# Performance work log

Measured on AMD Instinct MI355X. Metric: run time of the kernel, lower is better.

## Reference

```python
import jax, jax.numpy as jnp
import numpy as np

N = 50000   # nodes
E = 800000  # edges
D = 64      # num_filters == hidden_channels
NG = 5      # num_gaussians (edge_attr width, unused by forward math)
NEG_SLOPE = 0.2


def setup_inputs() -> dict:
    key = jax.random.key(0)
    ks = jax.random.split(key, 16)
    s = 1.0 / np.sqrt(D)
    return {
        "x": jax.random.normal(ks[0], (N, D), dtype=jnp.float32),
        "edge_index": jax.random.randint(ks[1], (2, E), 0, N, dtype=jnp.int64),
        "edge_weight": jax.random.uniform(ks[2], (E,), dtype=jnp.float32),
        "edge_attr": jax.random.normal(ks[3], (E, NG), dtype=jnp.float32),
        "W0": jax.random.normal(ks[4], (D, D), dtype=jnp.float32) * s,
        "b0": jnp.zeros((D,), dtype=jnp.float32),
        "W1": jax.random.normal(ks[5], (D, D), dtype=jnp.float32) * s,
        "as1": jax.random.normal(ks[6], (D,), dtype=jnp.float32) * s,
        "ad1": jax.random.normal(ks[7], (D,), dtype=jnp.float32) * s,
        "b1": jnp.zeros((D,), dtype=jnp.float32),
        "W2": jax.random.normal(ks[8], (D, D), dtype=jnp.float32) * s,
        "as2": jax.random.normal(ks[9], (D,), dtype=jnp.float32) * s,
        "ad2": jax.random.normal(ks[10], (D,), dtype=jnp.float32) * s,
        "b2": jnp.zeros((D,), dtype=jnp.float32),
    }


def gat_layer(h, src, dst, W, a_src, a_dst, b):
    # PyG GATConv, heads=1, add_self_loops=False
    hx = h @ W  # [N, D]
    # per-node attention logits, gathered per edge (edge j->i: src=j, dst=i)
    alpha = (hx * a_src).sum(-1)[src] + (hx * a_dst).sum(-1)[dst]  # [E]
    alpha = jax.nn.leaky_relu(alpha, NEG_SLOPE)
    # segment softmax grouped by destination node
    m = jax.ops.segment_max(alpha, dst, num_segments=N)
    e = jnp.exp(alpha - m[dst])
    s = jax.ops.segment_sum(e, dst, num_segments=N)
    p = e / s[dst]  # [E]
    # scatter-add weighted source features
    out = jax.ops.segment_sum(hx[src] * p[:, None], dst, num_segments=N)
    return out + b


def reference(x, edge_index, edge_weight, edge_attr,
              W0, b0, W1, as1, ad1, b1, W2, as2, ad2, b2):
    # edge_weight / edge_attr are accepted but unused, as in the torch module
    src, dst = edge_index[0], edge_index[1]
    out = jax.nn.relu(x @ W0 + b0)
    out = out + jax.nn.relu(gat_layer(out, src, dst, W1, as1, ad1, b1))
    out = out + jax.nn.relu(gat_layer(out, src, dst, W2, as2, ad2, b2))
    return out
```

## Files before the change

kernel.cpp:

```cpp
#include <hip/hip_runtime.h>
#include <hip/hip_bf16.h>

#define DD 64
#define NEG_SLOPE 0.2f
#define HS 68
#define BSH 8
#define BN  256
#define NBMAX 256
#define NBLK 256
#define STAGE_CAP 6144

__device__ __forceinline__ unsigned short f2bf(float f)
{
    unsigned u = __float_as_uint(f);
    u += 0x7FFFu + ((u >> 16) & 1u);
    return (unsigned short)(u >> 16);
}

__device__ __forceinline__ int wave_incl_scan(int v, int lane)
{
#pragma unroll
    for (int off = 1; off < 64; off <<= 1) {
        int t = __shfl_up(v, off);
        if (lane >= off) v += t;
    }
    return v;
}

__global__ __launch_bounds__(256) void k1_count_mm(
    const int4* __restrict__ dst4, const int* __restrict__ dst,
    int* __restrict__ cnts, int NB, int E4, int E, int C4,
    const float* __restrict__ x,
    const float* __restrict__ W0, const float* __restrict__ b0,
    const float* __restrict__ W1,
    const float* __restrict__ a_src, const float* __restrict__ a_dst,
    float* __restrict__ h, ushort4* __restrict__ hxb4,
    float* __restrict__ sarr, float* __restrict__ darr, int n)
{
    __shared__ float Wsh[DD * DD];
    __shared__ float Hsh[DD * HS];
    int tid = threadIdx.x;

    if (blockIdx.x < NBLK) {
        int* lh = (int*)Wsh;
        int k = blockIdx.x;
        for (int i = tid; i < NB; i += 256) lh[i] = 0;
        __syncthreads();
        int i0 = k * C4, i1 = min(i0 + C4, E4);
        for (int i = i0 + tid; i < i1; i += 256) {
            int4 d = dst4[i];
            atomicAdd(&lh[d.x >> BSH], 1);
            atomicAdd(&lh[d.y >> BSH], 1);
            atomicAdd(&lh[d.z >> BSH], 1);
            atomicAdd(&lh[d.w >> BSH], 1);
        }
        if (k == NBLK - 1) {
            for (int e = E4 * 4 + tid; e < E; e += 256)
                atomicAdd(&lh[dst[e] >> BSH], 1);
        }
        __syncthreads();
        for (int i = tid; i < NB; i += 256) cnts[k * NB + i] = lh[i];
        return;
    }

    for (int i = tid * 4; i < DD * DD; i += 1024)
        *(float4*)&Wsh[i] = *(const float4*)&W0[i];

    int fg = tid & 15, ng = tid >> 4;
    int tile0 = (blockIdx.x - NBLK) * 64;
    for (int p = 0; p < 4; ++p) {
        int nl = p * 16 + ng, gn = tile0 + nl;
        if (gn < n)
            *(float4*)&Hsh[nl * HS + 4 * fg] = *(const float4*)&x[gn * DD + 4 * fg];
    }
    __syncthreads();

    float4 acc[4];
#pragma unroll
    for (int j = 0; j < 4; ++j) acc[j] = float4{0.f, 0.f, 0.f, 0.f};
#pragma unroll 8
    for (int k = 0; k < DD; ++k) {
        float4 w4 = *(float4*)&Wsh[k * DD + 4 * fg];
#pragma unroll
        for (int j = 0; j < 4; ++j) {
            float hv = Hsh[(4 * ng + j) * HS + k];
            acc[j].x += hv * w4.x; acc[j].y += hv * w4.y;
            acc[j].z += hv * w4.z; acc[j].w += hv * w4.w;
        }
    }

    float4 b4 = *(const float4*)&b0[4 * fg];
    float4 o[4];
#pragma unroll
    for (int j = 0; j < 4; ++j) {
        o[j].x = fmaxf(acc[j].x + b4.x, 0.f);
        o[j].y = fmaxf(acc[j].y + b4.y, 0.f);
        o[j].z = fmaxf(acc[j].z + b4.z, 0.f);
        o[j].w = fmaxf(acc[j].w + b4.w, 0.f);
        int gn = tile0 + 4 * ng + j;
        if (gn < n) *(float4*)&h[gn * DD + 4 * fg] = o[j];
    }
    __syncthreads();

#pragma unroll
    for (int j = 0; j < 4; ++j)
        *(float4*)&Hsh[(4 * ng + j) * HS + 4 * fg] = o[j];
    for (int i = tid * 4; i < DD * DD; i += 1024)
        *(float4*)&Wsh[i] = *(const float4*)&W1[i];
    __syncthreads();

#pragma unroll
    for (int j = 0; j < 4; ++j) acc[j] = float4{0.f, 0.f, 0.f, 0.f};
#pragma unroll 8
    for (int k = 0; k < DD; ++k) {
        float4 w4 = *(float4*)&Wsh[k * DD + 4 * fg];
#pragma unroll
        for (int j = 0; j < 4; ++j) {
            float hv = Hsh[(4 * ng + j) * HS + k];
            acc[j].x += hv * w4.x; acc[j].y += hv * w4.y;
            acc[j].z += hv * w4.z; acc[j].w += hv * w4.w;
        }
    }

    float4 as4 = *(const float4*)&a_src[4 * fg];
    float4 ad4 = *(const float4*)&a_dst[4 * fg];
#pragma unroll
    for (int j = 0; j < 4; ++j) {
        int gn = tile0 + 4 * ng + j;
        if (gn < n) {
            ushort4 hb;
            hb.x = f2bf(acc[j].x); hb.y = f2bf(acc[j].y);
            hb.z = f2bf(acc[j].z); hb.w = f2bf(acc[j].w);
            hxb4[gn * 16 + fg] = hb;
        }
        float ps = acc[j].x * as4.x + acc[j].y * as4.y + acc[j].z * as4.z + acc[j].w * as4.w;
        float pd = acc[j].x * ad4.x + acc[j].y * ad4.y + acc[j].z * ad4.z + acc[j].w * ad4.w;
#pragma unroll
        for (int off = 8; off; off >>= 1) {
            ps += __shfl_xor(ps, off);
            pd += __shfl_xor(pd, off);
        }
        if (fg == 0 && gn < n) { sarr[gn] = ps; darr[gn] = pd; }
    }
}

__global__ __launch_bounds__(256) void mm_gat(
    const float* __restrict__ h, const float* __restrict__ W,
    const float* __restrict__ a_src, const float* __restrict__ a_dst,
    ushort4* __restrict__ hxb4, float* __restrict__ sarr, float* __restrict__ darr,
    int n)
{
    __shared__ float Wsh[DD * DD];
    __shared__ float Hsh[DD * HS];
    int tid = threadIdx.x;
    for (int i = tid * 4; i < DD * DD; i += 1024)
        *(float4*)&Wsh[i] = *(const float4*)&W[i];

    int fg = tid & 15, ng = tid >> 4;
    int tile0 = blockIdx.x * 64;
    for (int p = 0; p < 4; ++p) {
        int nl = p * 16 + ng, gn = tile0 + nl;
        if (gn < n)
            *(float4*)&Hsh[nl * HS + 4 * fg] = *(const float4*)&h[gn * DD + 4 * fg];
    }
    __syncthreads();

    float4 acc[4];
#pragma unroll
    for (int j = 0; j < 4; ++j) acc[j] = float4{0.f, 0.f, 0.f, 0.f};
#pragma unroll 8
    for (int k = 0; k < DD; ++k) {
        float4 w4 = *(float4*)&Wsh[k * DD + 4 * fg];
#pragma unroll
        for (int j = 0; j < 4; ++j) {
            float hv = Hsh[(4 * ng + j) * HS + k];
            acc[j].x += hv * w4.x; acc[j].y += hv * w4.y;
            acc[j].z += hv * w4.z; acc[j].w += hv * w4.w;
        }
    }

    float4 as4 = *(const float4*)&a_src[4 * fg];
    float4 ad4 = *(const float4*)&a_dst[4 * fg];
#pragma unroll
    for (int j = 0; j < 4; ++j) {
        int gn = tile0 + 4 * ng + j;
        if (gn < n) {
            ushort4 hb;
            hb.x = f2bf(acc[j].x); hb.y = f2bf(acc[j].y);
            hb.z = f2bf(acc[j].z); hb.w = f2bf(acc[j].w);
            hxb4[gn * 16 + fg] = hb;
        }
        float ps = acc[j].x * as4.x + acc[j].y * as4.y + acc[j].z * as4.z + acc[j].w * as4.w;
        float pd = acc[j].x * ad4.x + acc[j].y * ad4.y + acc[j].z * ad4.z + acc[j].w * ad4.w;
#pragma unroll
        for (int off = 8; off; off >>= 1) {
            ps += __shfl_xor(ps, off);
            pd += __shfl_xor(pd, off);
        }
        if (fg == 0 && gn < n) { sarr[gn] = ps; darr[gn] = pd; }
    }
}

__global__ __launch_bounds__(512) void k2_scan_scatter(
    const int* __restrict__ cnts,
    const int4* __restrict__ dst4, const int4* __restrict__ src4,
    const int* __restrict__ dst, const int* __restrict__ src,
    int* __restrict__ boff, int* __restrict__ row_ptr, int* __restrict__ ebuf,
    int NB, int N, int E, int E4, int C4)
{
    __shared__ int lcur[NBMAX];
    __shared__ int stot[NBMAX];
    __shared__ int wsum[4];
    int k = blockIdx.x, tid = threadIdx.x;

    int mybase = 0, tot = 0;
    if (tid < NB) {
        for (int kk = 0; kk < NBLK; ++kk) {
            int c = cnts[kk * NB + tid];
            tot += c;
            mybase += (kk < k) ? c : 0;
        }
        stot[tid] = tot;
    }
    __syncthreads();

    int lane = tid & 63, w = tid >> 6;
    int incl = 0, v = 0;
    if (tid < 256) {
        v = (tid < NB) ? stot[tid] : 0;
        incl = wave_incl_scan(v, lane);
        if (lane == 63) wsum[w] = incl;
    }
    __syncthreads();
    if (tid < NB) {
        int wo = 0;
        for (int i = 0; i < w; ++i) wo += wsum[i];
        int excl = wo + incl - v;
        lcur[tid] = excl + mybase;
        if (k == 0) {
            boff[tid] = excl;
            if (tid == 0) { boff[NB] = E; row_ptr[N] = E; }
        }
    }
    __syncthreads();

    int i0 = k * C4, i1 = min(i0 + C4, E4);
    for (int i = i0 + tid; i < i1; i += 512) {
        int4 d = dst4[i];
        int4 s = src4[i];
        int b, p;
        b = d.x >> BSH; p = atomicAdd(&lcur[b], 1); ebuf[p] = ((d.x & (BN - 1)) << 24) | s.x;
        b = d.y >> BSH; p = atomicAdd(&lcur[b], 1); ebuf[p] = ((d.y & (BN - 1)) << 24) | s.y;
        b = d.z >> BSH; p = atomicAdd(&lcur[b], 1); ebuf[p] = ((d.z & (BN - 1)) << 24) | s.z;
        b = d.w >> BSH; p = atomicAdd(&lcur[b], 1); ebuf[p] = ((d.w & (BN - 1)) << 24) | s.w;
    }
    if (k == NBLK - 1) {
        for (int e = E4 * 4 + tid; e < E; e += 512) {
            int d = dst[e];
            int b = d >> BSH;
            int p = atomicAdd(&lcur[b], 1);
            ebuf[p] = ((d & (BN - 1)) << 24) | src[e];
        }
    }
}

__global__ __launch_bounds__(512) void group_build(
    const int* __restrict__ ebuf, const int* __restrict__ boff,
    int* __restrict__ row_ptr, int* __restrict__ col, int N)
{
    __shared__ int lcnt[BN];
    __shared__ int loff[BN];
    __shared__ int lcur[BN];
    __shared__ int wsum[4];
    __shared__ int stage[STAGE_CAP];
    int b = blockIdx.x, tid = threadIdx.x;
    int e0 = boff[b], e1 = boff[b + 1];
    int total = e1 - e0;
    if (tid < BN) { lcnt[tid] = 0; lcur[tid] = 0; }
    __syncthreads();
    for (int e = e0 + tid; e < e1; e += 512)
        atomicAdd(&lcnt[((unsigned)ebuf[e]) >> 24], 1);
    __syncthreads();
    int lane = tid & 63, w = tid >> 6;
    int v = (tid < BN) ? lcnt[tid] : 0;
    int incl = wave_incl_scan(v, lane);
    if (tid < BN && lane == 63) wsum[w] = incl;
    __syncthreads();
    if (tid < BN) {
        int wo = 0;
        for (int i = 0; i < w; ++i) wo += wsum[i];
        int excl = wo + incl - v;
        loff[tid] = excl;
        int node = b * BN + tid;
        if (node < N) row_ptr[node] = e0 + excl;
    }
    __syncthreads();
    if (total <= STAGE_CAP) {
        for (int e = e0 + tid; e < e1; e += 512) {
            int p = ebuf[e];
            int dl = ((unsigned)p) >> 24;
            int r = atomicAdd(&lcur[dl], 1);
            stage[loff[dl] + r] = p & 0xFFFFFF;
        }
        __syncthreads();
        for (int i = tid; i < total; i += 512)
            col[e0 + i] = stage[i];
    } else {
        for (int e = e0 + tid; e < e1; e += 512) {
            int p = ebuf[e];
            int dl = ((unsigned)p) >> 24;
            int r = atomicAdd(&lcur[dl], 1);
            col[e0 + loff[dl] + r] = p & 0xFFFFFF;
        }
    }
}

__device__ __forceinline__ void agg_node(
    int node, int deg, const int* __restrict__ colp,
    const uint4* __restrict__ hxq, const float* __restrict__ sarr,
    float adi, const float* __restrict__ bias, float* __restrict__ h,
    int lane, int fl, int es)
{
    float acc[8];
#pragma unroll
    for (int j = 0; j < 8; ++j) acc[j] = 0.f;
    float inv = 0.f;

    if (deg > 0 && deg <= 64) {
        int c = 0; float a = -3.4e38f;
        if (lane < deg) {
            c = colp[lane];
            a = sarr[c] + adi;
            a = a > 0.f ? a : NEG_SLOPE * a;
        }
        float m = a;
#pragma unroll
        for (int off = 32; off; off >>= 1) m = fmaxf(m, __shfl_xor(m, off));
        float wgt = (lane < deg) ? __expf(a - m) : 0.f;
        float s = wgt;
#pragma unroll
        for (int off = 32; off; off >>= 1) s += __shfl_xor(s, off);
        inv = 1.f / s;

        for (int base = 0; base < deg; base += 8) {
            int e = base + es;
            float we = __shfl(wgt, e);
            int ce = __shfl(c, e);
            if (we > 0.f) {
                uint4 u = hxq[(size_t)ce * 8 + fl];
                acc[0] += we * __uint_as_float(u.x << 16);
                acc[1] += we * __uint_as_float(u.x & 0xffff0000u);
                acc[2] += we * __uint_as_float(u.y << 16);
                acc[3] += we * __uint_as_float(u.y & 0xffff0000u);
                acc[4] += we * __uint_as_float(u.z << 16);
                acc[5] += we * __uint_as_float(u.z & 0xffff0000u);
                acc[6] += we * __uint_as_float(u.w << 16);
                acc[7] += we * __uint_as_float(u.w & 0xffff0000u);
            }
        }
#pragma unroll
        for (int off = 8; off < 64; off <<= 1) {
#pragma unroll
            for (int j = 0; j < 8; ++j) acc[j] += __shfl_xor(acc[j], off);
        }
    } else if (deg > 64) {
        float m = -3.4e38f, s = 0.f;
        for (int e = es; e < deg; e += 8) {
            int cc = colp[e];
            float a = sarr[cc] + adi;
            a = a > 0.f ? a : NEG_SLOPE * a;
            uint4 u = hxq[(size_t)cc * 8 + fl];
            float mN = fmaxf(m, a);
            float f = __expf(m - mN);
            float wg = __expf(a - mN);
            m = mN; s = s * f + wg;
            acc[0] = acc[0] * f + wg * __uint_as_float(u.x << 16);
            acc[1] = acc[1] * f + wg * __uint_as_float(u.x & 0xffff0000u);
            acc[2] = acc[2] * f + wg * __uint_as_float(u.y << 16);
            acc[3] = acc[3] * f + wg * __uint_as_float(u.y & 0xffff0000u);
            acc[4] = acc[4] * f + wg * __uint_as_float(u.z << 16);
            acc[5] = acc[5] * f + wg * __uint_as_float(u.z & 0xffff0000u);
            acc[6] = acc[6] * f + wg * __uint_as_float(u.w << 16);
            acc[7] = acc[7] * f + wg * __uint_as_float(u.w & 0xffff0000u);
        }
#pragma unroll
        for (int off = 8; off < 64; off <<= 1) {
            float m2 = __shfl_xor(m, off);
            float s2 = __shfl_xor(s, off);
            float mN = fmaxf(m, m2);
            float f1 = __expf(m - mN);
            float f2 = __expf(m2 - mN);
            s = s * f1 + s2 * f2;
#pragma unroll
            for (int j = 0; j < 8; ++j) {
                float a2 = __shfl_xor(acc[j], off);
                acc[j] = acc[j] * f1 + a2 * f2;
            }
            m = mN;
        }
        inv = (s > 0.f) ? 1.f / s : 0.f;
    }

    if (es == 0) {
        float* hp = &h[(size_t)node * DD + fl * 8];
        float4 c0 = *(float4*)hp;
        float4 c1 = *(float4*)(hp + 4);
        const float* bp = &bias[fl * 8];
        float4 b0 = *(const float4*)bp;
        float4 b1 = *(const float4*)(bp + 4);
        c0.x += fmaxf(acc[0] * inv + b0.x, 0.f);
        c0.y += fmaxf(acc[1] * inv + b0.y, 0.f);
        c0.z += fmaxf(acc[2] * inv + b0.z, 0.f);
        c0.w += fmaxf(acc[3] * inv + b0.w, 0.f);
        c1.x += fmaxf(acc[4] * inv + b1.x, 0.f);
        c1.y += fmaxf(acc[5] * inv + b1.y, 0.f);
        c1.z += fmaxf(acc[6] * inv + b1.z, 0.f);
        c1.w += fmaxf(acc[7] * inv + b1.w, 0.f);
        *(float4*)hp = c0;
        *(float4*)(hp + 4) = c1;
    }
}

__global__ __launch_bounds__(256) void aggregate(
    const uint4* __restrict__ hxq, const int* __restrict__ row_ptr,
    const int* __restrict__ col, const float* __restrict__ sarr,
    const float* __restrict__ darr, const float* __restrict__ bias,
    float* __restrict__ h, int n)
{
    int tid = threadIdx.x;
    int wid = tid >> 6, lane = tid & 63;
    int fl = lane & 7, es = lane >> 3;
    int v = blockIdx.x * 4 + wid;
    if (v >= n) return;
    int beg = row_ptr[v], end = row_ptr[v + 1];
    agg_node(v, end - beg, &col[beg], hxq, sarr, darr[v], bias, h, lane, fl, es);
}

extern "C" void kernel_launch(void* const* d_in, const int* in_sizes, int n_in,
                              void* d_out, int out_size, void* d_ws, size_t ws_size,
                              hipStream_t stream)
{
    const float* x  = (const float*)d_in[0];
    const int*   ei = (const int*)d_in[1];
    const float* W0 = (const float*)d_in[4];
    const float* b0 = (const float*)d_in[5];
    const float* W1 = (const float*)d_in[6];
    const float* as1= (const float*)d_in[7];
    const float* ad1= (const float*)d_in[8];
    const float* b1 = (const float*)d_in[9];
    const float* W2 = (const float*)d_in[10];
    const float* as2= (const float*)d_in[11];
    const float* ad2= (const float*)d_in[12];
    const float* b2 = (const float*)d_in[13];

    int N = in_sizes[0] / DD;
    int E = in_sizes[1] / 2;
    int E4 = E >> 2;
    int C4 = (E4 + NBLK - 1) / NBLK;
    int NB = (N + BN - 1) >> BSH;
    float* h = (float*)d_out;

    ushort4* hxb4 = (ushort4*)d_ws;
    float* sarr   = (float*)(hxb4 + (size_t)N * 16);
    float* darr   = sarr + N;
    int*   row_ptr= (int*)(darr + N);
    int*   cnts   = row_ptr + (N + 1);
    int*   boff   = cnts + NBLK * NB;
    int*   ebuf   = boff + (NB + 1);
    int*   colb   = ebuf + E;

    const int* src = ei;
    const int* dst = ei + E;
    const int4* dst4 = (const int4*)dst;
    const int4* src4 = (const int4*)src;

    int mm_tiles = (N + 63) / 64;
    int agg_blks = (N + 3) / 4;

    k1_count_mm<<<NBLK + mm_tiles, 256, 0, stream>>>(
        dst4, dst, cnts, NB, E4, E, C4,
        x, W0, b0, W1, as1, ad1, h, hxb4, sarr, darr, N);

    k2_scan_scatter<<<NBLK, 512, 0, stream>>>(
        cnts, dst4, src4, dst, src, boff, row_ptr, ebuf, NB, N, E, E4, C4);

    group_build<<<NB, 512, 0, stream>>>(ebuf, boff, row_ptr, colb, N);

    aggregate<<<agg_blks, 256, 0, stream>>>(
        (const uint4*)hxb4, row_ptr, colb, sarr, darr, b1, h, N);

    mm_gat<<<mm_tiles, 256, 0, stream>>>(h, W2, as2, ad2, hxb4, sarr, darr, N);
    aggregate<<<agg_blks, 256, 0, stream>>>(
        (const uint4*)hxb4, row_ptr, colb, sarr, darr, b2, h, N);
}
```

Before: 219.8 us.

## Quantize transformed node features to int8 with per-node scale for aggregation

The bf16 copy of the transformed features gathered per edge is replaced with int8 values plus one float scale per node, which halves the bytes fetched for each edge in the gather-heavy aggregation. The aggregation lane mapping changes to 16 edges by 4 feature lanes, with per-edge weights pre-multiplied by the source scale. The matmul inner loop is also restructured to use float4 LDS reads over k. The cost is lower precision, with int8 quantisation error that could exceed tolerance, plus extra shuffle-max and rounding work in the producer kernels.

```diff
diff --git a/kernel.cpp b/kernel.cpp
--- a/kernel.cpp
+++ b/kernel.cpp
@@ -10,13 +10,6 @@
 #define NBLK 256
 #define STAGE_CAP 6144
 
-__device__ __forceinline__ unsigned short f2bf(float f)
-{
-    unsigned u = __float_as_uint(f);
-    u += 0x7FFFu + ((u >> 16) & 1u);
-    return (unsigned short)(u >> 16);
-}
-
 __device__ __forceinline__ int wave_incl_scan(int v, int lane)
 {
 #pragma unroll
@@ -26,6 +19,40 @@
     }
     return v;
 }
+
+__device__ __forceinline__ void quant_store(
+    float4 a, int gn, int fg, unsigned* __restrict__ hxq8u,
+    float* __restrict__ scl, int n)
+{
+    float amax = fmaxf(fmaxf(fabsf(a.x), fabsf(a.y)), fmaxf(fabsf(a.z), fabsf(a.w)));
+#pragma unroll
+    for (int off = 1; off < 16; off <<= 1) amax = fmaxf(amax, __shfl_xor(amax, off));
+    float iq = (amax > 0.f) ? 127.f / amax : 0.f;
+    int q0 = (int)rintf(a.x * iq), q1 = (int)rintf(a.y * iq);
+    int q2 = (int)rintf(a.z * iq), q3 = (int)rintf(a.w * iq);
+    unsigned u = (q0 & 255) | ((q1 & 255) << 8) | ((q2 & 255) << 16) | ((q3 & 255) << 24);
+    if (gn < n) {
+        hxq8u[(size_t)gn * 16 + fg] = u;
+        if (fg == 0) scl[gn] = amax * (1.f / 127.f);
+    }
+}
+
+#define MM_INNER(ACC)                                                         \
+    _Pragma("unroll")                                                         \
+    for (int k4 = 0; k4 < DD / 4; ++k4) {                                     \
+        float4 w0 = *(float4*)&Wsh[(4 * k4 + 0) * DD + 4 * fg];               \
+        float4 w1 = *(float4*)&Wsh[(4 * k4 + 1) * DD + 4 * fg];               \
+        float4 w2 = *(float4*)&Wsh[(4 * k4 + 2) * DD + 4 * fg];               \
+        float4 w3 = *(float4*)&Wsh[(4 * k4 + 3) * DD + 4 * fg];               \
+        _Pragma("unroll")                                                     \
+        for (int j = 0; j < 4; ++j) {                                         \
+            float4 hv = *(float4*)&Hsh[(4 * ng + j) * HS + 4 * k4];           \
+            ACC[j].x += hv.x * w0.x + hv.y * w1.x + hv.z * w2.x + hv.w * w3.x;\
+            ACC[j].y += hv.x * w0.y + hv.y * w1.y + hv.z * w2.y + hv.w * w3.y;\
+            ACC[j].z += hv.x * w0.z + hv.y * w1.z + hv.z * w2.z + hv.w * w3.z;\
+            ACC[j].w += hv.x * w0.w + hv.y * w1.w + hv.z * w2.w + hv.w * w3.w;\
+        }                                                                     \
+    }
 
 __global__ __launch_bounds__(256) void k1_count_mm(
     const int4* __restrict__ dst4, const int* __restrict__ dst,
@@ -34,7 +61,7 @@
     const float* __restrict__ W0, const float* __restrict__ b0,
     const float* __restrict__ W1,
     const float* __restrict__ a_src, const float* __restrict__ a_dst,
-    float* __restrict__ h, ushort4* __restrict__ hxb4,
+    float* __restrict__ h, unsigned* __restrict__ hxq8u, float* __restrict__ scl,
     float* __restrict__ sarr, float* __restrict__ darr, int n)
 {
     __shared__ float Wsh[DD * DD];
@@ -78,16 +105,7 @@
     float4 acc[4];
 #pragma unroll
     for (int j = 0; j < 4; ++j) acc[j] = float4{0.f, 0.f, 0.f, 0.f};
-#pragma unroll 8
-    for (int k = 0; k < DD; ++k) {
-        float4 w4 = *(float4*)&Wsh[k * DD + 4 * fg];
-#pragma unroll
-        for (int j = 0; j < 4; ++j) {
-            float hv = Hsh[(4 * ng + j) * HS + k];
-            acc[j].x += hv * w4.x; acc[j].y += hv * w4.y;
-            acc[j].z += hv * w4.z; acc[j].w += hv * w4.w;
-        }
-    }
+    MM_INNER(acc)
 
     float4 b4 = *(const float4*)&b0[4 * fg];
     float4 o[4];
@@ -111,28 +129,14 @@
 
 #pragma unroll
     for (int j = 0; j < 4; ++j) acc[j] = float4{0.f, 0.f, 0.f, 0.f};
-#pragma unroll 8
-    for (int k = 0; k < DD; ++k) {
-        float4 w4 = *(float4*)&Wsh[k * DD + 4 * fg];
-#pragma unroll
-        for (int j = 0; j < 4; ++j) {
-            float hv = Hsh[(4 * ng + j) * HS + k];
-            acc[j].x += hv * w4.x; acc[j].y += hv * w4.y;
-            acc[j].z += hv * w4.z; acc[j].w += hv * w4.w;
-        }
-    }
+    MM_INNER(acc)
 
     float4 as4 = *(const float4*)&a_src[4 * fg];
     float4 ad4 = *(const float4*)&a_dst[4 * fg];
 #pragma unroll
     for (int j = 0; j < 4; ++j) {
         int gn = tile0 + 4 * ng + j;
-        if (gn < n) {
-            ushort4 hb;
-            hb.x = f2bf(acc[j].x); hb.y = f2bf(acc[j].y);
-            hb.z = f2bf(acc[j].z); hb.w = f2bf(acc[j].w);
-            hxb4[gn * 16 + fg] = hb;
-        }
+        quant_store(acc[j], gn, fg, hxq8u, scl, n);
         float ps = acc[j].x * as4.x + acc[j].y * as4.y + acc[j].z * as4.z + acc[j].w * as4.w;
         float pd = acc[j].x * ad4.x + acc[j].y * ad4.y + acc[j].z * ad4.z + acc[j].w * ad4.w;
 #pragma unroll
@@ -147,8 +151,8 @@
 __global__ __launch_bounds__(256) void mm_gat(
     const float* __restrict__ h, const float* __restrict__ W,
     const float* __restrict__ a_src, const float* __restrict__ a_dst,
-    ushort4* __restrict__ hxb4, float* __restrict__ sarr, float* __restrict__ darr,
-    int n)
+    unsigned* __restrict__ hxq8u, float* __restrict__ scl,
+    float* __restrict__ sarr, float* __restrict__ darr, int n)
 {
     __shared__ float Wsh[DD * DD];
     __shared__ float Hsh[DD * HS];
@@ -168,28 +172,14 @@
     float4 acc[4];
 #pragma unroll
     for (int j = 0; j < 4; ++j) acc[j] = float4{0.f, 0.f, 0.f, 0.f};
-#pragma unroll 8
-    for (int k = 0; k < DD; ++k) {
-        float4 w4 = *(float4*)&Wsh[k * DD + 4 * fg];
-#pragma unroll
-        for (int j = 0; j < 4; ++j) {
-            float hv = Hsh[(4 * ng + j) * HS + k];
-            acc[j].x += hv * w4.x; acc[j].y += hv * w4.y;
-            acc[j].z += hv * w4.z; acc[j].w += hv * w4.w;
-        }
-    }
+    MM_INNER(acc)
 
     float4 as4 = *(const float4*)&a_src[4 * fg];
     float4 ad4 = *(const float4*)&a_dst[4 * fg];
 #pragma unroll
     for (int j = 0; j < 4; ++j) {
         int gn = tile0 + 4 * ng + j;
-        if (gn < n) {
-            ushort4 hb;
-            hb.x = f2bf(acc[j].x); hb.y = f2bf(acc[j].y);
-            hb.z = f2bf(acc[j].z); hb.w = f2bf(acc[j].w);
-            hxb4[gn * 16 + fg] = hb;
-        }
+        quant_store(acc[j], gn, fg, hxq8u, scl, n);
         float ps = acc[j].x * as4.x + acc[j].y * as4.y + acc[j].z * as4.z + acc[j].w * as4.w;
         float pd = acc[j].x * ad4.x + acc[j].y * ad4.y + acc[j].z * ad4.z + acc[j].w * ad4.w;
 #pragma unroll
@@ -317,13 +307,14 @@
 
 __device__ __forceinline__ void agg_node(
     int node, int deg, const int* __restrict__ colp,
-    const uint4* __restrict__ hxq, const float* __restrict__ sarr,
-    float adi, const float* __restrict__ bias, float* __restrict__ h,
-    int lane, int fl, int es)
-{
-    float acc[8];
-#pragma unroll
-    for (int j = 0; j < 8; ++j) acc[j] = 0.f;
+    const uint4* __restrict__ hxq8, const float* __restrict__ scl,
+    const float* __restrict__ sarr, float adi,
+    const float* __restrict__ bias, float* __restrict__ h, int lane)
+{
+    int fl = lane & 3, es = lane >> 2;
+    float acc[16];
+#pragma unroll
+    for (int i = 0; i < 16; ++i) acc[i] = 0.f;
     float inv = 0.f;
 
     if (deg > 0 && deg <= 64) {
@@ -341,50 +332,71 @@
 #pragma unroll
         for (int off = 32; off; off >>= 1) s += __shfl_xor(s, off);
         inv = 1.f / s;
-
-        for (int base = 0; base < deg; base += 8) {
+        float wsc = (lane < deg) ? wgt * scl[c] : 0.f;
+
+        for (int base = 0; base < deg; base += 16) {
             int e = base + es;
-            float we = __shfl(wgt, e);
-            int ce = __shfl(c, e);
-            if (we > 0.f) {
-                uint4 u = hxq[(size_t)ce * 8 + fl];
-                acc[0] += we * __uint_as_float(u.x << 16);
-                acc[1] += we * __uint_as_float(u.x & 0xffff0000u);
-                acc[2] += we * __uint_as_float(u.y << 16);
-                acc[3] += we * __uint_as_float(u.y & 0xffff0000u);
-                acc[4] += we * __uint_as_float(u.z << 16);
-                acc[5] += we * __uint_as_float(u.z & 0xffff0000u);
-                acc[6] += we * __uint_as_float(u.w << 16);
-                acc[7] += we * __uint_as_float(u.w & 0xffff0000u);
+            float bw = __shfl(wsc, e);
+            int bc = __shfl(c, e);
+            if (bw != 0.f) {
+                uint4 u = hxq8[(size_t)bc * 4 + fl];
+                int t;
+                t = (int)(u.x << 24) >> 24; acc[0]  += bw * (float)t;
+                t = (int)(u.x << 16) >> 24; acc[1]  += bw * (float)t;
+                t = (int)(u.x <<  8) >> 24; acc[2]  += bw * (float)t;
+                t = (int)u.x >> 24;         acc[3]  += bw * (float)t;
+                t = (int)(u.y << 24) >> 24; acc[4]  += bw * (float)t;
+                t = (int)(u.y << 16) >> 24; acc[5]  += bw * (float)t;
+                t = (int)(u.y <<  8) >> 24; acc[6]  += bw * (float)t;
+                t = (int)u.y >> 24;         acc[7]  += bw * (float)t;
+                t = (int)(u.z << 24) >> 24; acc[8]  += bw * (float)t;
+                t = (int)(u.z << 16) >> 24; acc[9]  += bw * (float)t;
+                t = (int)(u.z <<  8) >> 24; acc[10] += bw * (float)t;
+                t = (int)u.z >> 24;         acc[11] += bw * (float)t;
+                t = (int)(u.w << 24) >> 24; acc[12] += bw * (float)t;
+                t = (int)(u.w << 16) >> 24; acc[13] += bw * (float)t;
+                t = (int)(u.w <<  8) >> 24; acc[14] += bw * (float)t;
+                t = (int)u.w >> 24;         acc[15] += bw * (float)t;
             }
         }
 #pragma unroll
-        for (int off = 8; off < 64; off <<= 1) {
-#pragma unroll
-            for (int j = 0; j < 8; ++j) acc[j] += __shfl_xor(acc[j], off);
+        for (int off = 4; off < 64; off <<= 1) {
+#pragma unroll
+            for (int i = 0; i < 16; ++i) acc[i] += __shfl_xor(acc[i], off);
         }
     } else if (deg > 64) {
         float m = -3.4e38f, s = 0.f;
-        for (int e = es; e < deg; e += 8) {
-            int cc = colp[e];
-            float a = sarr[cc] + adi;
+        for (int e = es; e < deg; e += 16) {
+            int c = colp[e];
+            float a = sarr[c] + adi;
             a = a > 0.f ? a : NEG_SLOPE * a;
-            uint4 u = hxq[(size_t)cc * 8 + fl];
+            float sc = scl[c];
+            uint4 u = hxq8[(size_t)c * 4 + fl];
             float mN = fmaxf(m, a);
             float f = __expf(m - mN);
             float wg = __expf(a - mN);
             m = mN; s = s * f + wg;
-            acc[0] = acc[0] * f + wg * __uint_as_float(u.x << 16);
-            acc[1] = acc[1] * f + wg * __uint_as_float(u.x & 0xffff0000u);
-            acc[2] = acc[2] * f + wg * __uint_as_float(u.y << 16);
-            acc[3] = acc[3] * f + wg * __uint_as_float(u.y & 0xffff0000u);
-            acc[4] = acc[4] * f + wg * __uint_as_float(u.z << 16);
-            acc[5] = acc[5] * f + wg * __uint_as_float(u.z & 0xffff0000u);
-            acc[6] = acc[6] * f + wg * __uint_as_float(u.w << 16);
-            acc[7] = acc[7] * f + wg * __uint_as_float(u.w & 0xffff0000u);
-        }
-#pragma unroll
-        for (int off = 8; off < 64; off <<= 1) {
+            float wq = wg * sc;
+            int t;
+            t = (int)(u.x << 24) >> 24; acc[0]  = acc[0]  * f + wq * (float)t;
+            t = (int)(u.x << 16) >> 24; acc[1]  = acc[1]  * f + wq * (float)t;
+            t = (int)(u.x <<  8) >> 24; acc[2]  = acc[2]  * f + wq * (float)t;
+            t = (int)u.x >> 24;         acc[3]  = acc[3]  * f + wq * (float)t;
+            t = (int)(u.y << 24) >> 24; acc[4]  = acc[4]  * f + wq * (float)t;
+            t = (int)(u.y << 16) >> 24; acc[5]  = acc[5]  * f + wq * (float)t;
+            t = (int)(u.y <<  8) >> 24; acc[6]  = acc[6]  * f + wq * (float)t;
+            t = (int)u.y >> 24;         acc[7]  = acc[7]  * f + wq * (float)t;
+            t = (int)(u.z << 24) >> 24; acc[8]  = acc[8]  * f + wq * (float)t;
+            t = (int)(u.z << 16) >> 24; acc[9]  = acc[9]  * f + wq * (float)t;
+            t = (int)(u.z <<  8) >> 24; acc[10] = acc[10] * f + wq * (float)t;
+            t = (int)u.z >> 24;         acc[11] = acc[11] * f + wq * (float)t;
+            t = (int)(u.w << 24) >> 24; acc[12] = acc[12] * f + wq * (float)t;
+            t = (int)(u.w << 16) >> 24; acc[13] = acc[13] * f + wq * (float)t;
+            t = (int)(u.w <<  8) >> 24; acc[14] = acc[14] * f + wq * (float)t;
+            t = (int)u.w >> 24;         acc[15] = acc[15] * f + wq * (float)t;
+        }
+#pragma unroll
+        for (int off = 4; off < 64; off <<= 1) {
             float m2 = __shfl_xor(m, off);
             float s2 = __shfl_xor(s, off);
             float mN = fmaxf(m, m2);
@@ -392,9 +404,9 @@
             float f2 = __expf(m2 - mN);
             s = s * f1 + s2 * f2;
 #pragma unroll
-            for (int j = 0; j < 8; ++j) {
-                float a2 = __shfl_xor(acc[j], off);
-                acc[j] = acc[j] * f1 + a2 * f2;
+            for (int i = 0; i < 16; ++i) {
+                float a2 = __shfl_xor(acc[i], off);
+                acc[i] = acc[i] * f1 + a2 * f2;
             }
             m = mN;
         }
@@ -402,38 +414,33 @@
     }
 
     if (es == 0) {
-        float* hp = &h[(size_t)node * DD + fl * 8];
-        float4 c0 = *(float4*)hp;
-        float4 c1 = *(float4*)(hp + 4);
-        const float* bp = &bias[fl * 8];
-        float4 b0 = *(const float4*)bp;
-        float4 b1 = *(const float4*)(bp + 4);
-        c0.x += fmaxf(acc[0] * inv + b0.x, 0.f);
-        c0.y += fmaxf(acc[1] * inv + b0.y, 0.f);
-        c0.z += fmaxf(acc[2] * inv + b0.z, 0.f);
-        c0.w += fmaxf(acc[3] * inv + b0.w, 0.f);
-        c1.x += fmaxf(acc[4] * inv + b1.x, 0.f);
-        c1.y += fmaxf(acc[5] * inv + b1.y, 0.f);
-        c1.z += fmaxf(acc[6] * inv + b1.z, 0.f);
-        c1.w += fmaxf(acc[7] * inv + b1.w, 0.f);
-        *(float4*)hp = c0;
-        *(float4*)(hp + 4) = c1;
+        float* hp = &h[(size_t)node * DD + fl * 16];
+        const float* bp = &bias[fl * 16];
+#pragma unroll
+        for (int q = 0; q < 4; ++q) {
+            float4 cur = *(float4*)(hp + 4 * q);
+            float4 bb = *(const float4*)(bp + 4 * q);
+            cur.x += fmaxf(acc[4 * q + 0] * inv + bb.x, 0.f);
+            cur.y += fmaxf(acc[4 * q + 1] * inv + bb.y, 0.f);
+            cur.z += fmaxf(acc[4 * q + 2] * inv + bb.z, 0.f);
+            cur.w += fmaxf(acc[4 * q + 3] * inv + bb.w, 0.f);
+            *(float4*)(hp + 4 * q) = cur;
+        }
     }
 }
 
 __global__ __launch_bounds__(256) void aggregate(
-    const uint4* __restrict__ hxq, const int* __restrict__ row_ptr,
-    const int* __restrict__ col, const float* __restrict__ sarr,
-    const float* __restrict__ darr, const float* __restrict__ bias,
-    float* __restrict__ h, int n)
+    const uint4* __restrict__ hxq8, const float* __restrict__ scl,
+    const int* __restrict__ row_ptr, const int* __restrict__ col,
+    const float* __restrict__ sarr, const float* __restrict__ darr,
+    const float* __restrict__ bias, float* __restrict__ h, int n)
 {
     int tid = threadIdx.x;
     int wid = tid >> 6, lane = tid & 63;
-    int fl = lane & 7, es = lane >> 3;
     int v = blockIdx.x * 4 + wid;
     if (v >= n) return;
     int beg = row_ptr[v], end = row_ptr[v + 1];
-    agg_node(v, end - beg, &col[beg], hxq, sarr, darr[v], bias, h, lane, fl, es);
+    agg_node(v, end - beg, &col[beg], hxq8, scl, sarr, darr[v], bias, h, lane);
 }
 
 extern "C" void kernel_launch(void* const* d_in, const int* in_sizes, int n_in,
@@ -460,8 +467,9 @@
     int NB = (N + BN - 1) >> BSH;
     float* h = (float*)d_out;
 
-    ushort4* hxb4 = (ushort4*)d_ws;
-    float* sarr   = (float*)(hxb4 + (size_t)N * 16);
+    unsigned* hxq8u = (unsigned*)d_ws;
+    float* scl    = (float*)(hxq8u + (size_t)N * 16);
+    float* sarr   = scl + N;
     float* darr   = sarr + N;
     int*   row_ptr= (int*)(darr + N);
     int*   cnts   = row_ptr + (N + 1);
@@ -479,7 +487,7 @@
 
     k1_count_mm<<<NBLK + mm_tiles, 256, 0, stream>>>(
         dst4, dst, cnts, NB, E4, E, C4,
-        x, W0, b0, W1, as1, ad1, h, hxb4, sarr, darr, N);
+        x, W0, b0, W1, as1, ad1, h, hxq8u, scl, sarr, darr, N);
 
     k2_scan_scatter<<<NBLK, 512, 0, stream>>>(
         cnts, dst4, src4, dst, src, boff, row_ptr, ebuf, NB, N, E, E4, C4);
@@ -487,9 +495,9 @@
     group_build<<<NB, 512, 0, stream>>>(ebuf, boff, row_ptr, colb, N);
 
     aggregate<<<agg_blks, 256, 0, stream>>>(
-        (const uint4*)hxb4, row_ptr, colb, sarr, darr, b1, h, N);
-
-    mm_gat<<<mm_tiles, 256, 0, stream>>>(h, W2, as2, ad2, hxb4, sarr, darr, N);
+        (const uint4*)hxq8u, scl, row_ptr, colb, sarr, darr, b1, h, N);
+
+    mm_gat<<<mm_tiles, 256, 0, stream>>>(h, W2, as2, ad2, hxq8u, scl, sarr, darr, N);
     aggregate<<<agg_blks, 256, 0, stream>>>(
-        (const uint4*)hxb4, row_ptr, colb, sarr, darr, b2, h, N);
-}
+        (const uint4*)hxq8u, scl, row_ptr, colb, sarr, darr, b2, h, N);
+}
```

New measurement: 312.1 us. 1.42x slower.
